# Kernel tuning notes

Measured on AMD Instinct MI355X. Metric: run time of the kernel, lower is better.

## Reference

```python
import jax, jax.numpy as jnp
import numpy as np

B, C, H, W = 8, 64, 128, 128
O = 64
KH = KW = 3
K2 = KH * KW
STRIDE, PAD, DIL = 1, 1, 1


def setup_inputs() -> dict:
    key = jax.random.key(0)
    k1, k2, k3 = jax.random.split(key, 3)
    x = jax.random.normal(k1, (B, C, H, W), dtype=jnp.float32)
    # main deform-conv weight, fan-in scaled
    weight = jax.random.normal(k2, (O, C, KH, KW), dtype=jnp.float32) * (1.0 / np.sqrt(C * K2))
    # 1x1 offset conv; scaled small so offsets are a few pixels (original zero-init degenerates)
    w_off = jax.random.normal(k3, (2 * K2, C), dtype=jnp.float32) * 0.1
    b_off = jnp.zeros((2 * K2,), dtype=jnp.float32)
    return {"x": x, "weight": weight, "w_off": w_off, "b_off": b_off}


def _deform_conv(x, weight, w_off, b_off):
    Ho = (H + 2 * PAD - (DIL * (KH - 1) + 1)) // STRIDE + 1
    Wo = (W + 2 * PAD - (DIL * (KW - 1) + 1)) // STRIDE + 1
    # 1x1 offset conv -> [B, 2*K2, Ho, Wo] (stride 1 so Ho=H)
    off = jnp.einsum('bchw,oc->bohw', x, w_off) + b_off[None, :, None, None]
    off = off.reshape(B, K2, 2, Ho, Wo)
    off_y, off_x = off[:, :, 0], off[:, :, 1]  # [B, K2, Ho, Wo]

    kidx = jnp.arange(K2)
    kh = (kidx // KW).astype(jnp.float32)[None, :, None, None]
    kw = (kidx % KW).astype(jnp.float32)[None, :, None, None]
    gy = (jnp.arange(Ho, dtype=jnp.float32) * STRIDE - PAD)[None, None, :, None]
    gx = (jnp.arange(Wo, dtype=jnp.float32) * STRIDE - PAD)[None, None, None, :]
    py = gy + kh * DIL + off_y  # [B, K2, Ho, Wo]
    px = gx + kw * DIL + off_x

    y0 = jnp.floor(py)
    x0 = jnp.floor(px)
    wy1 = py - y0
    wx1 = px - x0
    wy0 = 1.0 - wy1
    wx0 = 1.0 - wx1

    def gather(yi, xi):
        valid = (yi >= 0) & (yi < H) & (xi >= 0) & (xi < W)
        yc = jnp.clip(yi, 0, H - 1).astype(jnp.int32)
        xc = jnp.clip(xi, 0, W - 1).astype(jnp.int32)
        # per-batch fancy gather: [C, K2, Ho, Wo]
        vals = jax.vmap(lambda xb, yb, xcb: xb[:, yb, xcb])(x, yc, xc)
        return vals * valid[:, None].astype(x.dtype)

    sampled = (gather(y0, x0) * (wy0 * wx0)[:, None]
               + gather(y0, x0 + 1) * (wy0 * wx1)[:, None]
               + gather(y0 + 1, x0) * (wy1 * wx0)[:, None]
               + gather(y0 + 1, x0 + 1) * (wy1 * wx1)[:, None])  # [B, C, K2, Ho, Wo]

    w = weight.reshape(O, C, K2)
    return jnp.einsum('bckhw,ock->bohw', sampled, w)


def reference(x, weight, w_off, b_off):
    return _deform_conv(x, weight, w_off, b_off)
```

## Files before the change

### kernel.cpp

```cpp
#include <hip/hip_runtime.h>

#define Bn 8
#define Cn 64
#define Hn 128
#define Wn 128
#define On 64
#define K2n 9
#define HWn (Hn * Wn)
#define OLP 20

typedef short bf16x8 __attribute__((ext_vector_type(8)));
typedef float f32x4  __attribute__((ext_vector_type(4)));

__device__ __forceinline__ unsigned f2bf(float f) {
    unsigned u = __float_as_uint(f);
    return (u + 0x7FFFu + ((u >> 16) & 1u)) >> 16;
}
__device__ __forceinline__ unsigned pkbf(float lo, float hi) {
    return f2bf(lo) | (f2bf(hi) << 16);
}
__device__ __forceinline__ float bflo(unsigned u) { return __uint_as_float(u << 16); }
__device__ __forceinline__ float bfhi(unsigned u) { return __uint_as_float(u & 0xFFFF0000u); }

__device__ __forceinline__ unsigned pkbf2(float lo, float hi) {
    const unsigned rlo = __float_as_uint(lo) + 0x8000u;
    const unsigned rhi = __float_as_uint(hi) + 0x8000u;
    return __builtin_amdgcn_perm(rhi, rlo, 0x07060302u);
}

__global__ __launch_bounds__(256) void prep_kernel(
        const float* __restrict__ x,
        const float* __restrict__ w,
        const float* __restrict__ w_off,
        unsigned* __restrict__ xT,
        unsigned short* __restrict__ wt2,
        unsigned short* __restrict__ woffr) {
    const int tid = threadIdx.x;
    const int bid = blockIdx.x;

    if (bid >= 2048) {
        int i = (bid - 2048) * 256 + tid;
        if (i < K2n * On * Cn) {
            int j    = i & 7;
            int lane = (i >> 3) & 63;
            int slot = i >> 9;
            int t  = slot & 3;
            int ks = (slot >> 2) & 1;
            int k  = slot >> 3;
            int o  = t * 16 + (lane & 15);
            int c  = ks * 32 + (lane >> 4) * 8 + j;
            wt2[i] = (unsigned short)f2bf(w[o * (Cn * K2n) + c * K2n + k]);
        } else {
            int idx  = i - K2n * On * Cn;
            int j    = idx & 7;
            int lane = (idx >> 3) & 63;
            int slot = idx >> 9;
            int t  = slot & 1;
            int ks = slot >> 1;
            int o  = t * 16 + (lane & 15);
            int c  = ks * 32 + (lane >> 4) * 8 + j;
            woffr[idx] = (o < 18) ? (unsigned short)f2bf(w_off[o * Cn + c]) : 0;
        }
        return;
    }

    __shared__ float tile[64 * 65];
    const int b   = bid >> 8;
    const int px0 = (bid & 255) << 6;

    {
        const int c = tid >> 2, pq = tid & 3;
        const float4* xp4 = (const float4*)(x + (size_t)b * (Cn * HWn)
                                              + (size_t)c * HWn + px0 + pq * 16);
        float4 v[4];
#pragma unroll
        for (int i = 0; i < 4; i++) v[i] = xp4[i];
#pragma unroll
        for (int i = 0; i < 16; i++)
            tile[(pq * 16 + i) * 65 + c] = (&v[0].x)[i];
    }
    __syncthreads();
    {
        const int c2 = tid & 31, r = tid >> 5;
        unsigned* dst = xT + ((size_t)b * HWn + px0) * 32;
#pragma unroll
        for (int j = 0; j < 8; j++) {
            const int p = j * 8 + r;
            dst[p * 32 + c2] = pkbf(tile[p * 65 + c2 * 2], tile[p * 65 + c2 * 2 + 1]);
        }
    }
}

struct Tap { float w00, w01, w10, w11; int c00, c01, c10, c11; };

__device__ __forceinline__ Tap mktap(int k, float offy, float offx, int h, int w) {
    Tap s;
    const int kh = k / 3, kw = k - kh * 3;
    const float py  = (float)(h - 1 + kh) + offy;
    const float pxf = (float)(w - 1 + kw) + offx;
    const float y0f = floorf(py), x0f = floorf(pxf);
    const float wy1 = py - y0f, wx1 = pxf - x0f;
    const float wy0 = 1.f - wy1, wx0 = 1.f - wx1;
    const int y0 = (int)y0f, x0i = (int)x0f;
    const int y1 = y0 + 1,  x1 = x0i + 1;
    const float zy0 = ((unsigned)y0  < (unsigned)Hn) ? wy0 : 0.f;
    const float zy1 = ((unsigned)y1  < (unsigned)Hn) ? wy1 : 0.f;
    const float zx0 = ((unsigned)x0i < (unsigned)Wn) ? wx0 : 0.f;
    const float zx1 = ((unsigned)x1  < (unsigned)Wn) ? wx1 : 0.f;
    s.w00 = zy0 * zx0; s.w01 = zy0 * zx1;
    s.w10 = zy1 * zx0; s.w11 = zy1 * zx1;
    const int yc0 = min(max(y0, 0), Hn - 1), yc1 = min(max(y1, 0), Hn - 1);
    const int xc0 = min(max(x0i, 0), Wn - 1), xc1 = min(max(x1, 0), Wn - 1);
    s.c00 = (yc0 * Wn + xc0) * 32; s.c01 = (yc0 * Wn + xc1) * 32;
    s.c10 = (yc1 * Wn + xc0) * 32; s.c11 = (yc1 * Wn + xc1) * 32;
    return s;
}

__device__ __forceinline__ void combine4(unsigned* dst, const uint4* u, const Tap& s) {
#pragma unroll
    for (int i = 0; i < 4; i++) {
        const unsigned a = (&u[0].x)[i], b = (&u[1].x)[i];
        const unsigned c = (&u[2].x)[i], d = (&u[3].x)[i];
        const float slo = s.w00 * bflo(a) + s.w01 * bflo(b)
                        + s.w10 * bflo(c) + s.w11 * bflo(d);
        const float shi = s.w00 * bfhi(a) + s.w01 * bfhi(b)
                        + s.w10 * bfhi(c) + s.w11 * bfhi(d);
        dst[i] = pkbf2(slo, shi);
    }
}

__device__ __forceinline__ void gather8(uint4* u, const unsigned* xb,
                                        const Tap& s, int c2) {
    const unsigned* g00 = xb + s.c00 + c2 * 4;
    const unsigned* g01 = xb + s.c01 + c2 * 4;
    const unsigned* g10 = xb + s.c10 + c2 * 4;
    const unsigned* g11 = xb + s.c11 + c2 * 4;
    u[0] = *(const uint4*)g00;
    u[1] = *(const uint4*)g01;
    u[2] = *(const uint4*)g10;
    u[3] = *(const uint4*)g11;
    u[4] = *(const uint4*)(g00 + 16);
    u[5] = *(const uint4*)(g01 + 16);
    u[6] = *(const uint4*)(g10 + 16);
    u[7] = *(const uint4*)(g11 + 16);
}

__global__ __launch_bounds__(256, 2) void dcn_kernel(
        const unsigned* __restrict__ xT,
        const unsigned short* __restrict__ wt2,
        const unsigned short* __restrict__ woffr,
        const float* __restrict__ b_off,
        float* __restrict__ out) {
    __shared__ __align__(16) unsigned shmem[4][2][16 * 36];
    __shared__ __align__(16) unsigned short wtl[2][8 * 512];
    float* const offl = (float*)&shmem[0][0][0];

    const int tid = threadIdx.x;
    const int bid = blockIdx.x;
    const int logical = ((bid & 7) << 8) | (bid >> 3);
    const int b   = logical >> 8;
    const int hw0 = (logical & 255) << 6;

    const int lane = tid & 63;
    const int wv   = tid >> 6;
    const int q    = lane >> 4;
    const int sp   = lane & 15;
    const int m    = lane >> 2;
    const int c2   = lane & 3;
    const int pix0 = hw0 + wv * 16;
    const int pix  = pix0 + sp;

    const unsigned* xb = xT + (size_t)b * (HWn * 32);

    {
        union { uint4 u; bf16x8 v; } aw0, aw1;
        aw0.u = *(const uint4*)(xb + pix * 32 + q * 4);
        aw1.u = *(const uint4*)(xb + pix * 32 + 16 + q * 4);
        f32x4 oa0 = (f32x4){0.f, 0.f, 0.f, 0.f};
        f32x4 oa1 = (f32x4){0.f, 0.f, 0.f, 0.f};
        const bf16x8 bo00 = *(const bf16x8*)(woffr + 0 * 512 + lane * 8);
        const bf16x8 bo01 = *(const bf16x8*)(woffr + 1 * 512 + lane * 8);
        const bf16x8 bo10 = *(const bf16x8*)(woffr + 2 * 512 + lane * 8);
        const bf16x8 bo11 = *(const bf16x8*)(woffr + 3 * 512 + lane * 8);
        oa0 = __builtin_amdgcn_mfma_f32_16x16x32_bf16(aw0.v, bo00, oa0, 0, 0, 0);
        oa1 = __builtin_amdgcn_mfma_f32_16x16x32_bf16(aw0.v, bo01, oa1, 0, 0, 0);
        oa0 = __builtin_amdgcn_mfma_f32_16x16x32_bf16(aw1.v, bo10, oa0, 0, 0, 0);
        oa1 = __builtin_amdgcn_mfma_f32_16x16x32_bf16(aw1.v, bo11, oa1, 0, 0, 0);
        const int oc = lane & 15, rg = lane >> 4;
        float* ol = offl + wv * (16 * OLP);
        const float bo_a = b_off[oc];
#pragma unroll
        for (int r = 0; r < 4; r++)
            ol[(rg * 4 + r) * OLP + oc] = oa0[r] + bo_a;
        if (oc < 2) {
            const float bo_b = b_off[16 + oc];
#pragma unroll
            for (int r = 0; r < 4; r++)
                ol[(rg * 4 + r) * OLP + 16 + oc] = oa1[r] + bo_b;
        }
    }
    {
        const uint4* s0 = (const uint4*)(wt2);
        uint4* d0 = (uint4*)(&wtl[0][0]);
        d0[tid]       = s0[tid];
        d0[tid + 256] = s0[tid + 256];
    }
    asm volatile("s_waitcnt lgkmcnt(0)" ::: "memory");

    const float* olp = offl + wv * (16 * OLP) + m * OLP;
    float off[18];
#pragma unroll
    for (int i = 0; i < 9; i++) {
        const float2 o2 = *(const float2*)(olp + 2 * i);
        off[2 * i]     = o2.x;
        off[2 * i + 1] = o2.y;
    }

    __syncthreads();

    const int pixm = pix0 + m;
    const int hm = pixm >> 7;
    const int wm = pixm & 127;
    unsigned* cwv = &shmem[wv][0][0];

    f32x4 acc[4];
#pragma unroll
    for (int t = 0; t < 4; t++) acc[t] = (f32x4){0.f, 0.f, 0.f, 0.f};

    uint4 u[2][8];
    Tap   tp[2];
    tp[0] = mktap(0, off[0], off[1], hm, wm);
    gather8(u[0], xb, tp[0], c2);

#pragma unroll
    for (int k = 0; k < K2n; k++) {
        const int cur = k & 1, nxt = cur ^ 1;

        if (k + 1 < K2n) {
            const uint4* sn = (const uint4*)(wt2 + (size_t)(k + 1) * 4096);
            uint4* dn = (uint4*)(&wtl[nxt][0]);
            dn[tid]       = sn[tid];
            dn[tid + 256] = sn[tid + 256];
            tp[nxt] = mktap(k + 1, off[2 * k + 2], off[2 * k + 3], hm, wm);
            gather8(u[nxt], xb, tp[nxt], c2);
        }

        unsigned A0[4], A1[4];
        combine4(A0, &u[cur][0], tp[cur]);
        combine4(A1, &u[cur][4], tp[cur]);

        unsigned* cb = cwv + cur * 576;
        *(uint4*)(cb + m * 36 + c2 * 4)      = make_uint4(A0[0], A0[1], A0[2], A0[3]);
        *(uint4*)(cb + m * 36 + 16 + c2 * 4) = make_uint4(A1[0], A1[1], A1[2], A1[3]);

        asm volatile("s_waitcnt lgkmcnt(0)" ::: "memory");

        const bf16x8 af0 = *(const bf16x8*)(cb + sp * 36 + q * 4);
        const bf16x8 af1 = *(const bf16x8*)(cb + sp * 36 + 16 + q * 4);

        const unsigned short* bl = &wtl[cur][lane * 8];
#pragma unroll
        for (int t = 0; t < 4; t++) {
            const bf16x8 b0 = *(const bf16x8*)(bl + t * 512);
            acc[t] = __builtin_amdgcn_mfma_f32_16x16x32_bf16(af0, b0, acc[t], 0, 0, 0);
            const bf16x8 b1 = *(const bf16x8*)(bl + (4 + t) * 512);
            acc[t] = __builtin_amdgcn_mfma_f32_16x16x32_bf16(af1, b1, acc[t], 0, 0, 0);
        }

        __syncthreads();
    }

    const int oc = lane & 15;
    const int rg = lane >> 4;
    float* ob = out + (size_t)b * (On * HWn) + pix0 + rg * 4;
#pragma unroll
    for (int t = 0; t < 4; t++) {
        const int o = t * 16 + oc;
        *(f32x4*)(ob + (size_t)o * HWn) = acc[t];
    }
}

extern "C" void kernel_launch(void* const* d_in, const int* in_sizes, int n_in,
                              void* d_out, int out_size, void* d_ws, size_t ws_size,
                              hipStream_t stream) {
    const float* x      = (const float*)d_in[0];
    const float* weight = (const float*)d_in[1];
    const float* w_off  = (const float*)d_in[2];
    const float* b_off  = (const float*)d_in[3];
    float* out = (float*)d_out;

    unsigned*       xT    = (unsigned*)d_ws;
    unsigned short* wt2   = (unsigned short*)((char*)d_ws + 16777216);
    unsigned short* woffr = (unsigned short*)((char*)d_ws + 16777216 + 73728);

    prep_kernel<<<2200, 256, 0, stream>>>(x, weight, w_off, xT, wt2, woffr);
    dcn_kernel<<<2048, 256, 0, stream>>>(xT, wt2, woffr, b_off, out);
}
```

Measured before the change: 124.1 us.

## Replace LDS staging with ds_bpermute and per-lane global weight loads

Removes the shared-memory staging of the combined bilinear samples and of the weight tiles. Each lane now reads its MFMA B fragments straight from global memory (cached), and A fragments are rearranged across lanes with ds_bpermute instead of a store/load round trip through LDS. This drops the per-tap __syncthreads and the block-wide weight copy, and shrinks LDS to the offset buffer. The cost is more global/L2 weight traffic per wave, extra registers for the 8 weight fragments, and 8 bpermutes per tap.

```diff
diff --git a/kernel.cpp b/kernel.cpp
--- a/kernel.cpp
+++ b/kernel.cpp
@@ -151,9 +151,7 @@
         const unsigned short* __restrict__ woffr,
         const float* __restrict__ b_off,
         float* __restrict__ out) {
-    __shared__ __align__(16) unsigned shmem[4][2][16 * 36];
-    __shared__ __align__(16) unsigned short wtl[2][8 * 512];
-    float* const offl = (float*)&shmem[0][0][0];
+    __shared__ float offl[4 * 16 * OLP];
 
     const int tid = threadIdx.x;
     const int bid = blockIdx.x;
@@ -165,8 +163,8 @@
     const int wv   = tid >> 6;
     const int q    = lane >> 4;
     const int sp   = lane & 15;
-    const int m    = lane >> 2;
-    const int c2   = lane & 3;
+    const int m    = (lane >> 1) & 15;
+    const int c2   = (lane & 1) | ((lane >> 4) & 2);
     const int pix0 = hw0 + wv * 16;
     const int pix  = pix0 + sp;
 
@@ -199,12 +197,6 @@
                 ol[(rg * 4 + r) * OLP + 16 + oc] = oa1[r] + bo_b;
         }
     }
-    {
-        const uint4* s0 = (const uint4*)(wt2);
-        uint4* d0 = (uint4*)(&wtl[0][0]);
-        d0[tid]       = s0[tid];
-        d0[tid + 256] = s0[tid + 256];
-    }
     asm volatile("s_waitcnt lgkmcnt(0)" ::: "memory");
 
     const float* olp = offl + wv * (16 * OLP) + m * OLP;
@@ -216,12 +208,11 @@
         off[2 * i + 1] = o2.y;
     }
 
-    __syncthreads();
-
     const int pixm = pix0 + m;
     const int hm = pixm >> 7;
     const int wm = pixm & 127;
-    unsigned* cwv = &shmem[wv][0][0];
+
+    const int bidx = ((lane & 32) | (sp << 1) | (q & 1)) << 2;
 
     f32x4 acc[4];
 #pragma unroll
@@ -237,37 +228,31 @@
         const int cur = k & 1, nxt = cur ^ 1;
 
         if (k + 1 < K2n) {
-            const uint4* sn = (const uint4*)(wt2 + (size_t)(k + 1) * 4096);
-            uint4* dn = (uint4*)(&wtl[nxt][0]);
-            dn[tid]       = sn[tid];
-            dn[tid + 256] = sn[tid + 256];
             tp[nxt] = mktap(k + 1, off[2 * k + 2], off[2 * k + 3], hm, wm);
             gather8(u[nxt], xb, tp[nxt], c2);
         }
+
+        const unsigned short* bp = wt2 + (size_t)(k * 8) * 512 + lane * 8;
+        bf16x8 wtr[8];
+#pragma unroll
+        for (int t = 0; t < 8; t++) wtr[t] = *(const bf16x8*)(bp + t * 512);
 
         unsigned A0[4], A1[4];
         combine4(A0, &u[cur][0], tp[cur]);
         combine4(A1, &u[cur][4], tp[cur]);
 
-        unsigned* cb = cwv + cur * 576;
-        *(uint4*)(cb + m * 36 + c2 * 4)      = make_uint4(A0[0], A0[1], A0[2], A0[3]);
-        *(uint4*)(cb + m * 36 + 16 + c2 * 4) = make_uint4(A1[0], A1[1], A1[2], A1[3]);
-
-        asm volatile("s_waitcnt lgkmcnt(0)" ::: "memory");
-
-        const bf16x8 af0 = *(const bf16x8*)(cb + sp * 36 + q * 4);
-        const bf16x8 af1 = *(const bf16x8*)(cb + sp * 36 + 16 + q * 4);
-
-        const unsigned short* bl = &wtl[cur][lane * 8];
+        union { unsigned w[4]; bf16x8 v; } f0, f1;
+#pragma unroll
+        for (int i = 0; i < 4; i++) {
+            f0.w[i] = (unsigned)__builtin_amdgcn_ds_bpermute(bidx, (int)A0[i]);
+            f1.w[i] = (unsigned)__builtin_amdgcn_ds_bpermute(bidx, (int)A1[i]);
+        }
+
 #pragma unroll
         for (int t = 0; t < 4; t++) {
-            const bf16x8 b0 = *(const bf16x8*)(bl + t * 512);
-            acc[t] = __builtin_amdgcn_mfma_f32_16x16x32_bf16(af0, b0, acc[t], 0, 0, 0);
-            const bf16x8 b1 = *(const bf16x8*)(bl + (4 + t) * 512);
-            acc[t] = __builtin_amdgcn_mfma_f32_16x16x32_bf16(af1, b1, acc[t], 0, 0, 0);
-        }
-
-        __syncthreads();
+            acc[t] = __builtin_amdgcn_mfma_f32_16x16x32_bf16(f0.v, wtr[t],     acc[t], 0, 0, 0);
+            acc[t] = __builtin_amdgcn_mfma_f32_16x16x32_bf16(f1.v, wtr[4 + t], acc[t], 0, 0, 0);
+        }
     }
 
     const int oc = lane & 15;
```

Measured after the change: 143.5 us. 15.7% more time.
